# Optimization experiments

Measured on AMD Instinct MI355X. Metric: run time of the kernel, lower is better.

The kernel has to match this reference:

```python
import jax, jax.numpy as jnp
import numpy as np

B, H, W, D, C, NH = 2, 32, 32, 32, 256, 8
LN_EPS = 1e-3  # keras LayerNormalization default epsilon


def _ln(x, g, b):
    m = jnp.mean(x, axis=-1, keepdims=True)
    v = jnp.mean(jnp.square(x - m), axis=-1, keepdims=True)
    return (x - m) * jax.lax.rsqrt(v + LN_EPS) * g + b


def setup_inputs() -> dict:
    key = jax.random.key(0)
    ks = jax.random.split(key, 8)
    w = lambda k, shape, fan: (jax.random.normal(k, shape, jnp.float32) / np.sqrt(fan)).astype(jnp.float32)
    return {
        "q": jax.random.normal(ks[0], (B, H, W, D, C), jnp.float32),
        "kv": jax.random.normal(ks[1], (B, H, W, D, C), jnp.float32),
        "wq_w": w(ks[2], (C, C), C), "wq_b": jnp.zeros((C,), jnp.float32),
        "wk_w": w(ks[3], (C, C), C), "wk_b": jnp.zeros((C,), jnp.float32),
        "wv_w": w(ks[4], (C, C), C), "wv_b": jnp.zeros((C,), jnp.float32),
        "ln1_g": jnp.ones((C,), jnp.float32), "ln1_b": jnp.zeros((C,), jnp.float32),
        "ff1_w": w(ks[5], (C, 4 * C), C), "ff1_b": jnp.zeros((4 * C,), jnp.float32),
        "ff2_w": w(ks[6], (4 * C, C), 4 * C), "ff2_b": jnp.zeros((C,), jnp.float32),
        "ln2_g": jnp.ones((C,), jnp.float32), "ln2_b": jnp.zeros((C,), jnp.float32),
    }


def reference(q, kv, wq_w, wq_b, wk_w, wk_b, wv_w, wv_b,
              ln1_g, ln1_b, ff1_w, ff1_b, ff2_w, ff2_b, ln2_g, ln2_b):
    Bq, Hh, Ww, Dd, Cc = q.shape
    dh = Cc // NH
    qf = q.reshape(Bq, -1, Cc)          # (B, N, C), N = H*W*D
    inq = qf
    kvf = kv.reshape(Bq, -1, Cc)

    def split_heads(x):                  # (B, N, C) -> (B, h, N, dh)
        return x.reshape(Bq, -1, NH, dh).transpose(0, 2, 1, 3)

    qh = split_heads(qf @ wq_w + wq_b)
    kh = split_heads(kvf @ wk_w + wk_b)
    vh = split_heads(kvf @ wv_w + wv_b)

    # efficient (linear) attention: softmax over N on k^T, softmax over dh on q
    k_norm = jax.nn.softmax(kh.transpose(0, 1, 3, 2), axis=-1)   # (B, h, dh, N)
    q_norm = jax.nn.softmax(qh, axis=-1)                         # (B, h, N, dh)
    context = jnp.einsum('bhdn,bhne->bhde', k_norm, vh)          # (B, h, dh, dh)
    attn = jnp.einsum('bhnd,bhde->bhne', q_norm, context)        # (B, h, N, dh)
    attn = attn.transpose(0, 2, 1, 3).reshape(Bq, -1, Cc)

    x = _ln(inq + attn, ln1_g, ln1_b)
    ff = jax.nn.gelu(x @ ff1_w + ff1_b, approximate=False) @ ff2_w + ff2_b
    out = _ln(x + ff, ln2_g, ln2_b)
    return out.reshape(Bq, Hh, Ww, Dd, Cc)
```

## Files before the change

### kernel.cpp

```cpp
#include <hip/hip_runtime.h>
#include <hip/hip_bf16.h>

#define NTOK_B   32768
#define TOK_TOT  65536
#define CDIM     256
#define NHEAD    8
#define DHEAD    32
#define FFDIM    1024
#define LN_EPS   1e-3f

typedef __attribute__((ext_vector_type(8))) short bf16x8;
typedef __attribute__((ext_vector_type(4))) float f32x4;

__device__ __forceinline__ float bf2f(short s) {
    union { unsigned u; float f; } v; v.u = ((unsigned)(unsigned short)s) << 16; return v.f;
}
__device__ __forceinline__ short f2bf(float f) {
    union { float f; unsigned u; } v; v.f = f;
    unsigned r = (v.u + 0x7FFFu + ((v.u >> 16) & 1u)) >> 16;
    return (short)r;
}

__device__ __forceinline__ void gld_lds16(const void* g, void* l) {
    __builtin_amdgcn_global_load_lds(
        (const __attribute__((address_space(1))) unsigned int*)g,
        (__attribute__((address_space(3))) unsigned int*)l, 16, 0, 0);
}

__global__ __launch_bounds__(256) void cast_bf16(const float* __restrict__ in,
                                                 short* __restrict__ out)
{
    long i = ((long)blockIdx.x * 256 + threadIdx.x) * 8;
    float4 a = *(const float4*)(in + i);
    float4 b = *(const float4*)(in + i + 4);
    short t[8];
    t[0] = f2bf(a.x); t[1] = f2bf(a.y); t[2] = f2bf(a.z); t[3] = f2bf(a.w);
    t[4] = f2bf(b.x); t[5] = f2bf(b.y); t[6] = f2bf(b.z); t[7] = f2bf(b.w);
    *(int4*)(out + i) = *(const int4*)t;
}

__global__ __launch_bounds__(256) void transpose_k(const float* __restrict__ in,
                                                   short* __restrict__ out, int K, int N)
{
    __shared__ float t[32][33];
    int kt = blockIdx.x * 32, nt = blockIdx.y * 32;
    int tx = threadIdx.x, ty = threadIdx.y;
#pragma unroll
    for (int i = 0; i < 4; ++i)
        t[ty + i * 8][tx] = in[(long)(kt + ty + i * 8) * N + nt + tx];
    __syncthreads();
#pragma unroll
    for (int i = 0; i < 4; ++i)
        out[(long)(nt + ty + i * 8) * K + kt + tx] = f2bf(t[tx][ty + i * 8]);
}

__global__ __launch_bounds__(256) void concat_bias(const float* __restrict__ a,
                                                   const float* __restrict__ b,
                                                   float* __restrict__ o)
{
    int i = blockIdx.x * 256 + threadIdx.x;
    o[i] = (i < 256) ? a[i] : b[i - 256];
}

template<int ACT, int NBX>
__global__ __launch_bounds__(256) void gemm_bt(const short* __restrict__ Xv,
                                               const short* __restrict__ Wt,
                                               const float* __restrict__ bias,
                                               short* __restrict__ Outp,
                                               int N, int K, int ldx, int ldo)
{
    constexpr int LOG2NBX = (NBX == 2) ? 1 : (NBX == 4) ? 2 : 3;
    __shared__ __align__(16) char smem[49152];
    short* As = (short*)smem;
    short* Bs = (short*)(smem + 24576);

    const int tid  = threadIdx.x;
    const int lane = tid & 63;
    const int wave = tid >> 6;
    const int wm   = (wave >> 1) * 4;
    const int wn   = (wave & 1) * 4;

    const int bid  = blockIdx.x;
    const int xcd  = bid & 7;
    const int j    = bid >> 3;
    const int nblk = j & (NBX - 1);
    const int mblk = xcd * 64 + (j >> LOG2NBX);
    const long m0  = (long)mblk * 128;
    const int  n0  = nblk * 128;

    f32x4 acc[4][4];
#pragma unroll
    for (int i = 0; i < 4; ++i)
#pragma unroll
        for (int jj = 0; jj < 4; ++jj) acc[i][jj] = (f32x4)0.0f;

    const int NT = K >> 5;

    auto stage = [&](int kt, int buf) {
#pragma unroll
        for (int p = 0; p < 2; ++p) {
            int idx = tid + p * 256;
            int row = (idx >> 6) * 16 + (idx & 15);
            int qq  = (idx >> 4) & 3;
            int lofs = buf * 4096 + (p * 256 + wave * 64) * 8;
            gld_lds16(Xv + (m0 + row) * (long)ldx + kt * 32 + qq * 8, As + lofs);
            gld_lds16(Wt + (long)(n0 + row) * K + kt * 32 + qq * 8,  Bs + lofs);
        }
    };

    stage(0, 0);
    if (NT > 1) stage(1, 1);
    int cb = 0;
    for (int kt = 0; kt < NT; ++kt) {
        __builtin_amdgcn_sched_barrier(0);
        if (kt + 1 < NT) asm volatile("s_waitcnt vmcnt(4)" ::: "memory");
        else             asm volatile("s_waitcnt vmcnt(0)" ::: "memory");
        __builtin_amdgcn_s_barrier();
        __builtin_amdgcn_sched_barrier(0);
        if (kt + 2 < NT) {
            int sb = cb + 2; if (sb >= 3) sb -= 3;
            stage(kt + 2, sb);
        }
        bf16x8 a[4], b[4];
#pragma unroll
        for (int i = 0; i < 4; ++i) a[i] = *(const bf16x8*)(As + cb * 4096 + ((wm + i) * 64 + lane) * 8);
#pragma unroll
        for (int jj = 0; jj < 4; ++jj) b[jj] = *(const bf16x8*)(Bs + cb * 4096 + ((wn + jj) * 64 + lane) * 8);
#pragma unroll
        for (int i = 0; i < 4; ++i)
#pragma unroll
            for (int jj = 0; jj < 4; ++jj)
                acc[i][jj] = __builtin_amdgcn_mfma_f32_16x16x32_bf16(a[i], b[jj], acc[i][jj], 0, 0, 0);
        cb = (cb + 1 == 3) ? 0 : cb + 1;
    }

    __syncthreads();
    short* Cs = (short*)smem;
    const int crow0 = (wave >> 1) * 64 + (lane >> 4) * 4;
    const int ccol0 = (wave & 1) * 64 + (lane & 15);
#pragma unroll
    for (int jj = 0; jj < 4; ++jj) {
        int colw = ccol0 + jj * 16;
        float bb = bias[n0 + colw];
#pragma unroll
        for (int i = 0; i < 4; ++i) {
#pragma unroll
            for (int r = 0; r < 4; ++r) {
                float v = acc[i][jj][r] + bb;
                if (ACT == 1) {
                    float w = -1.5957691216057308f * (v + 0.044715f * v * v * v);
                    v = v / (1.0f + __expf(w));
                }
                Cs[(crow0 + i * 16 + r) * 136 + colw] = f2bf(v);
            }
        }
    }
    __syncthreads();
#pragma unroll
    for (int it = 0; it < 8; ++it) {
        int ch = tid + it * 256;
        int row = ch >> 4, c8 = ch & 15;
        int4 v = *(const int4*)(Cs + row * 136 + c8 * 8);
        *(int4*)(Outp + (m0 + row) * (long)ldo + n0 + c8 * 8) = v;
    }
}

__global__ __launch_bounds__(256) void ff2_ln(const short* __restrict__ H,
                                              const short* __restrict__ Wt2,
                                              const float* __restrict__ b2f,
                                              const short* __restrict__ xbuf,
                                              const float* __restrict__ g2,
                                              const float* __restrict__ b2,
                                              float* __restrict__ y)
{
    __shared__ __align__(16) char smem[61440];

    const int tid  = threadIdx.x;
    const int lane = tid & 63;
    const int wave = tid >> 6;

    const int bid  = blockIdx.x;
    const int mblk = (bid & 7) * 128 + (bid >> 3);
    const long m0  = (long)mblk * 64;

    f32x4 acc[4][4];
#pragma unroll
    for (int i = 0; i < 4; ++i)
#pragma unroll
        for (int jj = 0; jj < 4; ++jj) acc[i][jj] = (f32x4)0.0f;

    auto stage = [&](int kt, int buf) {
        char* base = smem + buf * 20480;
        {
            int row = wave * 16 + (lane & 15);
            int qq  = lane >> 4;
            gld_lds16(H + (m0 + row) * 1024L + kt * 32 + qq * 8,
                      base + wave * 1024);
        }
#pragma unroll
        for (int p = 0; p < 4; ++p) {
            int ti  = p * 4 + wave;
            int row = ti * 16 + (lane & 15);
            int qq  = lane >> 4;
            gld_lds16(Wt2 + row * 1024L + kt * 32 + qq * 8,
                      base + 4096 + (p * 256 + wave * 64) * 16);
        }
    };

    const int NT = 32;
    stage(0, 0);
    stage(1, 1);
    int cb = 0;
    for (int kt = 0; kt < NT; ++kt) {
        __builtin_amdgcn_sched_barrier(0);
        if (kt + 1 < NT) asm volatile("s_waitcnt vmcnt(5)" ::: "memory");
        else             asm volatile("s_waitcnt vmcnt(0)" ::: "memory");
        __builtin_amdgcn_s_barrier();
        __builtin_amdgcn_sched_barrier(0);
        if (kt + 2 < NT) {
            int sb = cb + 2; if (sb >= 3) sb -= 3;
            stage(kt + 2, sb);
        }
        const short* Ab = (const short*)(smem + cb * 20480);
        const short* Bb = (const short*)(smem + cb * 20480 + 4096);
        bf16x8 a[4], b[4];
#pragma unroll
        for (int i = 0; i < 4; ++i) a[i] = *(const bf16x8*)(Ab + (i * 64 + lane) * 8);
#pragma unroll
        for (int jj = 0; jj < 4; ++jj) b[jj] = *(const bf16x8*)(Bb + ((wave * 4 + jj) * 64 + lane) * 8);
#pragma unroll
        for (int i = 0; i < 4; ++i)
#pragma unroll
            for (int jj = 0; jj < 4; ++jj)
                acc[i][jj] = __builtin_amdgcn_mfma_f32_16x16x32_bf16(a[i], b[jj], acc[i][jj], 0, 0, 0);
        cb = (cb + 1 == 3) ? 0 : cb + 1;
    }

    __syncthreads();
    float* red = (float*)smem;
    float* mr  = red + 512;

    float g2c[4], b2c[4], bfc[4];
#pragma unroll
    for (int jj = 0; jj < 4; ++jj) {
        int col = wave * 64 + (lane & 15) + jj * 16;
        bfc[jj] = b2f[col]; g2c[jj] = g2[col]; b2c[jj] = b2[col];
    }

#pragma unroll
    for (int i = 0; i < 4; ++i) {
#pragma unroll
        for (int r = 0; r < 4; ++r) {
            int row = i * 16 + (lane >> 4) * 4 + r;
            float s = 0.0f, ss = 0.0f;
#pragma unroll
            for (int jj = 0; jj < 4; ++jj) {
                int col = wave * 64 + (lane & 15) + jj * 16;
                float val = acc[i][jj][r] + bfc[jj]
                          + bf2f(xbuf[(m0 + row) * 256 + col]);
                acc[i][jj][r] = val;
                s += val; ss += val * val;
            }
            s  += __shfl_xor(s, 1);  ss += __shfl_xor(ss, 1);
            s  += __shfl_xor(s, 2);  ss += __shfl_xor(ss, 2);
            s  += __shfl_xor(s, 4);  ss += __shfl_xor(ss, 4);
            s  += __shfl_xor(s, 8);  ss += __shfl_xor(ss, 8);
            if ((lane & 15) == 0) {
                red[(row * 4 + wave) * 2]     = s;
                red[(row * 4 + wave) * 2 + 1] = ss;
            }
        }
    }
    __syncthreads();
    if (tid < 64) {
        float s  = red[tid * 8] + red[tid * 8 + 2] + red[tid * 8 + 4] + red[tid * 8 + 6];
        float ss = red[tid * 8 + 1] + red[tid * 8 + 3] + red[tid * 8 + 5] + red[tid * 8 + 7];
        float mean = s * (1.0f / 256.0f);
        float var  = ss * (1.0f / 256.0f) - mean * mean;
        mr[tid * 2]     = mean;
        mr[tid * 2 + 1] = rsqrtf(var + LN_EPS);
    }
    __syncthreads();
#pragma unroll
    for (int i = 0; i < 4; ++i) {
#pragma unroll
        for (int r = 0; r < 4; ++r) {
            int row = i * 16 + (lane >> 4) * 4 + r;
            float mean = mr[row * 2], rstd = mr[row * 2 + 1];
#pragma unroll
            for (int jj = 0; jj < 4; ++jj) {
                int col = wave * 64 + (lane & 15) + jj * 16;
                y[(m0 + row) * 256 + col] =
                    (acc[i][jj][r] - mean) * rstd * g2c[jj] + b2c[jj];
            }
        }
    }
}

#define CCH 512
#define CPS 64
__global__ __launch_bounds__(256) void context_k(const short* __restrict__ QKV,
                                                 float* __restrict__ ctx,
                                                 float* __restrict__ ksum)
{
    const int b = blockIdx.z, h = blockIdx.y;
    const long tokbase = (long)b * NTOK_B + (long)blockIdx.x * CCH;
    __shared__ __align__(16) float kb[2][CPS][32];
    __shared__ __align__(16) float vb[2][CPS][32];
    const int tid  = threadIdx.x;
    const int wave = tid >> 6;
    const int lane = tid & 63;
    const int t    = lane;
    const int koff = (wave < 2) ? 256 : 512;
    const int choff = (wave & 1) * 16;
    const short* src0 = QKV + (tokbase + t) * 768 + koff + h * 32 + choff;

    const int d2 = lane >> 2;
    const int eg = lane & 3;
    __align__(16) float acc[2][8];
#pragma unroll
    for (int i = 0; i < 2; ++i)
#pragma unroll
        for (int j = 0; j < 8; ++j) acc[i][j] = 0.0f;
    float s0 = 0.0f, s1 = 0.0f;

    int4 p0 = *(const int4*)src0;
    int4 p1 = *(const int4*)(src0 + 8);
    const int NP = CCH / CPS;
    for (int p = 0; p < NP; ++p) {
        int4 n0 = p0, n1 = p1;
        if (p + 1 < NP) {
            const short* sn = src0 + (long)(p + 1) * CPS * 768;
            n0 = *(const int4*)sn;
            n1 = *(const int4*)(sn + 8);
        }
        {
            short sh[16];
            *(int4*)&sh[0] = p0; *(int4*)&sh[8] = p1;
            float v[16];
            if (wave < 2) {
#pragma unroll
                for (int i = 0; i < 16; ++i) v[i] = __expf(bf2f(sh[i]));
            } else {
#pragma unroll
                for (int i = 0; i < 16; ++i) v[i] = bf2f(sh[i]);
            }
            char* rowp = (char*)((wave < 2) ? &kb[p & 1][t][0] : &vb[p & 1][t][0]);
            int sw = (t & 7) << 4;
#pragma unroll
            for (int q = 0; q < 4; ++q) {
                int qq = (choff >> 2) + q;
                *(float4*)(rowp + ((qq * 16) ^ sw)) =
                    make_float4(v[q * 4], v[q * 4 + 1], v[q * 4 + 2], v[q * 4 + 3]);
            }
        }
        __syncthreads();
        {
            const int buf = p & 1;
#pragma unroll
            for (int k = 0; k < 16; ++k) {
                int tt = wave * 16 + k;
                int sw = (tt & 7) << 4;
                const char* krow = (const char*)&kb[buf][tt][0];
                const char* vrow = (const char*)&vb[buf][tt][0];
                float2 kd = *(const float2*)(krow + ((d2 * 8) ^ sw));
                float4 va = *(const float4*)(vrow + ((eg * 32) ^ sw));
                float4 vbb = *(const float4*)(vrow + ((eg * 32 + 16) ^ sw));
                acc[0][0] += kd.x * va.x;  acc[0][1] += kd.x * va.y;
                acc[0][2] += kd.x * va.z;  acc[0][3] += kd.x * va.w;
                acc[0][4] += kd.x * vbb.x; acc[0][5] += kd.x * vbb.y;
                acc[0][6] += kd.x * vbb.z; acc[0][7] += kd.x * vbb.w;
                acc[1][0] += kd.y * va.x;  acc[1][1] += kd.y * va.y;
                acc[1][2] += kd.y * va.z;  acc[1][3] += kd.y * va.w;
                acc[1][4] += kd.y * vbb.x; acc[1][5] += kd.y * vbb.y;
                acc[1][6] += kd.y * vbb.z; acc[1][7] += kd.y * vbb.w;
                if (eg == 0) { s0 += kd.x; s1 += kd.y; }
            }
        }
        p0 = n0; p1 = n1;
    }

    __syncthreads();
    float* red = &kb[0][0][0];
    float* rs  = &vb[0][0][0];
#pragma unroll
    for (int dd = 0; dd < 2; ++dd) {
        *(float4*)&red[wave * 1024 + (d2 * 2 + dd) * 32 + eg * 8]     = *(float4*)&acc[dd][0];
        *(float4*)&red[wave * 1024 + (d2 * 2 + dd) * 32 + eg * 8 + 4] = *(float4*)&acc[dd][4];
    }
    if (eg == 0) { rs[wave * 32 + d2 * 2] = s0; rs[wave * 32 + d2 * 2 + 1] = s1; }
    __syncthreads();
    {
        float* cbase = ctx + ((long)(b * 8 + h) * 32) * 32;
        int i0 = tid * 4;
        float4 a  = *(float4*)&red[i0];
        float4 b4 = *(float4*)&red[1024 + i0];
        float4 c4 = *(float4*)&red[2048 + i0];
        float4 d4 = *(float4*)&red[3072 + i0];
        atomicAdd(cbase + i0 + 0, a.x + b4.x + c4.x + d4.x);
        atomicAdd(cbase + i0 + 1, a.y + b4.y + c4.y + d4.y);
        atomicAdd(cbase + i0 + 2, a.z + b4.z + c4.z + d4.z);
        atomicAdd(cbase + i0 + 3, a.w + b4.w + c4.w + d4.w);
        if (tid < 32) {
            float s = rs[tid] + rs[32 + tid] + rs[64 + tid] + rs[96 + tid];
            atomicAdd(ksum + b * 256 + h * 32 + tid, s);
        }
    }
}

__global__ __launch_bounds__(256) void attn_ln1(const short* __restrict__ QKV,
                                                const float* __restrict__ qin,
                                                const float* __restrict__ ctx,
                                                const float* __restrict__ ksum,
                                                const float* __restrict__ g1,
                                                const float* __restrict__ b1,
                                                short* __restrict__ xout)
{
    long tok0blk = (long)blockIdx.x * 128;
    int b = (int)(tok0blk >> 15);
    __shared__ __align__(16) float qn[16][292];
    __shared__ __align__(16) float xb[16][292];
    __shared__ float red[16][8][2];
    __shared__ float mr[16][2];
    int tid = threadIdx.x;
    int h = tid >> 5, e = tid & 31;

    float cregs[32];
    {
        const float* cp = ctx + ((long)(b * 8 + h) * 32) * 32 + e;
        const float* zs = ksum + b * 256 + h * 32;
#pragma unroll
        for (int d = 0; d < 32; ++d) cregs[d] = cp[d * 32] / zs[d];
    }

    for (int sub = 0; sub < 8; ++sub) {
        long tok0 = tok0blk + sub * 16;
        if (tid < 128) {
            int tA = tid >> 3, hA = tid & 7;
            const short* Qp = QKV + (tok0 + tA) * 768 + hA * 32;
            short qv[32];
            *(int4*)&qv[0]  = *(const int4*)(Qp);
            *(int4*)&qv[8]  = *(const int4*)(Qp + 8);
            *(int4*)&qv[16] = *(const int4*)(Qp + 16);
            *(int4*)&qv[24] = *(const int4*)(Qp + 24);
            float f[32]; float mx = -1e30f;
#pragma unroll
            for (int i = 0; i < 32; ++i) { f[i] = bf2f(qv[i]); mx = fmaxf(mx, f[i]); }
            float s = 0.0f;
#pragma unroll
            for (int i = 0; i < 32; ++i) { f[i] = __expf(f[i] - mx); s += f[i]; }
            float inv = 1.0f / s;
            float* qrow = &qn[tA][hA * 36];
#pragma unroll
            for (int i = 0; i < 32; ++i) qrow[i] = f[i] * inv;
        }
        __syncthreads();
        {
            int cch = h * 32 + e;
#pragma unroll 2
            for (int t = 0; t < 16; ++t) {
                const float4* qr = (const float4*)&qn[t][h * 36];
                float a = 0.0f;
#pragma unroll
                for (int d4 = 0; d4 < 8; ++d4) {
                    float4 qv = qr[d4];
                    a += qv.x * cregs[d4 * 4 + 0] + qv.y * cregs[d4 * 4 + 1]
                       + qv.z * cregs[d4 * 4 + 2] + qv.w * cregs[d4 * 4 + 3];
                }
                float iv = qin[(tok0 + t) * 256 + cch];
                xb[t][cch] = a + iv;
            }
        }
        __syncthreads();
        if (tid < 128) {
            int tC = tid & 15, sC = tid >> 4;
            float s = 0, ss = 0;
            const float* xr = &xb[tC][sC * 32];
#pragma unroll
            for (int i = 0; i < 32; ++i) { float v = xr[i]; s += v; ss += v * v; }
            red[tC][sC][0] = s; red[tC][sC][1] = ss;
        }
        __syncthreads();
        if (tid < 16) {
            float s = 0, ss = 0;
#pragma unroll
            for (int k = 0; k < 8; ++k) { s += red[tid][k][0]; ss += red[tid][k][1]; }
            float mean = s * (1.0f / 256.0f);
            float var  = ss * (1.0f / 256.0f) - mean * mean;
            mr[tid][0] = mean; mr[tid][1] = rsqrtf(var + LN_EPS);
        }
        __syncthreads();
        if (tid < 128) {
            int tC = tid & 15, sC = tid >> 4;
            float mean = mr[tC][0], rstd = mr[tC][1];
            const float* xr = &xb[tC][sC * 32];
            short ov[32];
#pragma unroll
            for (int i = 0; i < 32; ++i) {
                int c = sC * 32 + i;
                float v = (xr[i] - mean) * rstd * g1[c] + b1[c];
                ov[i] = f2bf(v);
            }
            int4* op = (int4*)(xout + (tok0 + tC) * 256 + sC * 32);
            op[0] = *(int4*)&ov[0];  op[1] = *(int4*)&ov[8];
            op[2] = *(int4*)&ov[16]; op[3] = *(int4*)&ov[24];
        }
        __syncthreads();
    }
}

extern "C" void kernel_launch(void* const* d_in, const int* in_sizes, int n_in,
                              void* d_out, int out_size, void* d_ws, size_t ws_size,
                              hipStream_t stream)
{
    const float* q    = (const float*)d_in[0];
    const float* kv   = (const float*)d_in[1];
    const float* wq_w = (const float*)d_in[2];
    const float* wq_b = (const float*)d_in[3];
    const float* wk_w = (const float*)d_in[4];
    const float* wk_b = (const float*)d_in[5];
    const float* wv_w = (const float*)d_in[6];
    const float* wv_b = (const float*)d_in[7];
    const float* ln1g = (const float*)d_in[8];
    const float* ln1b = (const float*)d_in[9];
    const float* ff1w = (const float*)d_in[10];
    const float* ff1b = (const float*)d_in[11];
    const float* ff2w = (const float*)d_in[12];
    const float* ff2b = (const float*)d_in[13];
    const float* ln2g = (const float*)d_in[14];
    const float* ln2b = (const float*)d_in[15];

    char* w = (char*)d_ws;
    short* Wtq = (short*)w; w += 131072;
    short* Wtk = (short*)w; w += 131072;
    short* Wtv = (short*)w; w += 131072;
    short* Wt1 = (short*)w; w += 524288;
    short* Wt2 = (short*)w; w += 524288;
    float* ksm = (float*)w; w += 2048;
    float* bkv = (float*)w; w += 2048;
    float* ctx = (float*)w; w += 65536;
    short* xbuf= (short*)w; w += 33554432;
    short* QKV = (short*)w; w += 134217728;
    short* kvb = (short*)w; w += 33554432;
    short* h1  = QKV;
    short* qb  = xbuf;
    float* y   = (float*)d_out;

    cast_bf16<<<8192, 256, 0, stream>>>(q,  qb);
    cast_bf16<<<8192, 256, 0, stream>>>(kv, kvb);

    dim3 tb(32, 8);
    transpose_k<<<dim3(8, 8),  tb, 0, stream>>>(wq_w, Wtq, 256, 256);
    transpose_k<<<dim3(8, 8),  tb, 0, stream>>>(wk_w, Wtk, 256, 256);
    transpose_k<<<dim3(8, 8),  tb, 0, stream>>>(wv_w, Wtv, 256, 256);
    transpose_k<<<dim3(8, 32), tb, 0, stream>>>(ff1w, Wt1, 256, 1024);
    transpose_k<<<dim3(32, 8), tb, 0, stream>>>(ff2w, Wt2, 1024, 256);
    concat_bias<<<2, 256, 0, stream>>>(wk_b, wv_b, bkv);

    gemm_bt<0,2><<<1024, 256, 0, stream>>>(qb,  Wtq, wq_b, QKV + 0,   256, 256, 256, 768);
    gemm_bt<0,4><<<2048, 256, 0, stream>>>(kvb, Wtk, bkv,  QKV + 256, 512, 256, 256, 768);

    hipMemsetAsync(ctx, 0, 65536, stream);
    hipMemsetAsync(ksm, 0, 2048, stream);
    context_k<<<dim3(NTOK_B / CCH, 8, 2), 256, 0, stream>>>(QKV, ctx, ksm);

    attn_ln1<<<512, 256, 0, stream>>>(QKV, q, ctx, ksm, ln1g, ln1b, xbuf);

    gemm_bt<1,8><<<4096, 256, 0, stream>>>(xbuf, Wt1, ff1b, h1, 1024, 256, 256, 1024);

    ff2_ln<<<1024, 256, 0, stream>>>(h1, Wt2, ff2b, xbuf, ln2g, ln2b, y);
}
```

Before: 570.5 us.

## Fuse FF1 GEMM, GELU, FF2 GEMM and LayerNorm into one kernel

```diff
diff --git a/kernel.cpp b/kernel.cpp
--- a/kernel.cpp
+++ b/kernel.cpp
@@ -25,6 +25,11 @@
     __builtin_amdgcn_global_load_lds(
         (const __attribute__((address_space(1))) unsigned int*)g,
         (__attribute__((address_space(3))) unsigned int*)l, 16, 0, 0);
+}
+
+__device__ __forceinline__ float fast_gelu(float v) {
+    float w = -1.5957691216057308f * (v + 0.044715f * v * v * v);
+    return v / (1.0f + __expf(w));
 }
 
 __global__ __launch_bounds__(256) void cast_bf16(const float* __restrict__ in,
@@ -147,10 +152,7 @@
 #pragma unroll
             for (int r = 0; r < 4; ++r) {
                 float v = acc[i][jj][r] + bb;
-                if (ACT == 1) {
-                    float w = -1.5957691216057308f * (v + 0.044715f * v * v * v);
-                    v = v / (1.0f + __expf(w));
-                }
+                if (ACT == 1) v = fast_gelu(v);
                 Cs[(crow0 + i * 16 + r) * 136 + colw] = f2bf(v);
             }
         }
@@ -165,85 +167,131 @@
     }
 }
 
-__global__ __launch_bounds__(256) void ff2_ln(const short* __restrict__ H,
-                                              const short* __restrict__ Wt2,
-                                              const float* __restrict__ b2f,
-                                              const short* __restrict__ xbuf,
-                                              const float* __restrict__ g2,
-                                              const float* __restrict__ b2,
-                                              float* __restrict__ y)
-{
-    __shared__ __align__(16) char smem[61440];
+__global__ __launch_bounds__(256, 2) void ffn_fused(const short* __restrict__ X,
+                                                    const short* __restrict__ W1t,
+                                                    const float* __restrict__ b1f,
+                                                    const short* __restrict__ W2t,
+                                                    const float* __restrict__ b2f,
+                                                    const short* __restrict__ xdummy,
+                                                    const float* __restrict__ g2,
+                                                    const float* __restrict__ b2,
+                                                    float* __restrict__ y)
+{
+    __shared__ __align__(16) short lds[40960];
+    short* Xs = lds;
+    short* Wb = lds + 16384;
+    short* hs = lds + 32768;
 
     const int tid  = threadIdx.x;
     const int lane = tid & 63;
-    const int wave = tid >> 6;
+    const int w    = tid >> 6;
 
     const int bid  = blockIdx.x;
     const int mblk = (bid & 7) * 128 + (bid >> 3);
     const long m0  = (long)mblk * 64;
 
-    f32x4 acc[4][4];
+    f32x4 yacc[4][4];
 #pragma unroll
     for (int i = 0; i < 4; ++i)
 #pragma unroll
-        for (int jj = 0; jj < 4; ++jj) acc[i][jj] = (f32x4)0.0f;
-
-    auto stage = [&](int kt, int buf) {
-        char* base = smem + buf * 20480;
-        {
-            int row = wave * 16 + (lane & 15);
-            int qq  = lane >> 4;
-            gld_lds16(H + (m0 + row) * 1024L + kt * 32 + qq * 8,
-                      base + wave * 1024);
-        }
+        for (int jj = 0; jj < 4; ++jj) yacc[i][jj] = (f32x4)0.0f;
+
+    {
+        int ti = (tid >> 6) & 3, q = (tid >> 4) & 3, m = tid & 15;
+        const short* gsrc = X + (m0 + ti * 16 + m) * 256 + q * 8;
+#pragma unroll
+        for (int it = 0; it < 8; ++it)
+            gld_lds16(gsrc + it * 32, Xs + it * 2048 + w * 512);
+    }
+
+    auto stageW1 = [&](int c, int s, int buf) {
+#pragma unroll
+        for (int p = 0; p < 2; ++p) {
+            int cc = p * 256 + tid;
+            int ti = cc >> 6, q = (cc >> 4) & 3, m = cc & 15;
+            gld_lds16(W1t + (c * 128 + ti * 16 + m) * 256 + s * 32 + q * 8,
+                      Wb + buf * 8192 + (p * 256 + w * 64) * 8);
+        }
+    };
+    auto stageW2 = [&](int c, int ks, int buf) {
 #pragma unroll
         for (int p = 0; p < 4; ++p) {
-            int ti  = p * 4 + wave;
-            int row = ti * 16 + (lane & 15);
-            int qq  = lane >> 4;
-            gld_lds16(Wt2 + row * 1024L + kt * 32 + qq * 8,
-                      base + 4096 + (p * 256 + wave * 64) * 16);
+            int cc = p * 256 + tid;
+            int ti = cc >> 6, q = (cc >> 4) & 3, m = cc & 15;
+            gld_lds16(W2t + (ti * 16 + m) * 1024 + c * 128 + ks * 32 + q * 8,
+                      Wb + buf * 8192 + (p * 256 + w * 64) * 8);
         }
     };
 
-    const int NT = 32;
-    stage(0, 0);
-    stage(1, 1);
-    int cb = 0;
-    for (int kt = 0; kt < NT; ++kt) {
-        __builtin_amdgcn_sched_barrier(0);
-        if (kt + 1 < NT) asm volatile("s_waitcnt vmcnt(5)" ::: "memory");
-        else             asm volatile("s_waitcnt vmcnt(0)" ::: "memory");
-        __builtin_amdgcn_s_barrier();
-        __builtin_amdgcn_sched_barrier(0);
-        if (kt + 2 < NT) {
-            int sb = cb + 2; if (sb >= 3) sb -= 3;
-            stage(kt + 2, sb);
-        }
-        const short* Ab = (const short*)(smem + cb * 20480);
-        const short* Bb = (const short*)(smem + cb * 20480 + 4096);
-        bf16x8 a[4], b[4];
-#pragma unroll
-        for (int i = 0; i < 4; ++i) a[i] = *(const bf16x8*)(Ab + (i * 64 + lane) * 8);
-#pragma unroll
-        for (int jj = 0; jj < 4; ++jj) b[jj] = *(const bf16x8*)(Bb + ((wave * 4 + jj) * 64 + lane) * 8);
-#pragma unroll
-        for (int i = 0; i < 4; ++i)
-#pragma unroll
-            for (int jj = 0; jj < 4; ++jj)
-                acc[i][jj] = __builtin_amdgcn_mfma_f32_16x16x32_bf16(a[i], b[jj], acc[i][jj], 0, 0, 0);
-        cb = (cb + 1 == 3) ? 0 : cb + 1;
-    }
-
-    __syncthreads();
-    float* red = (float*)smem;
+    stageW1(0, 0, 0);
+
+    f32x4 hacc[4][2];
+    float b1a = 0.0f, b1b = 0.0f;
+
+    for (int c = 0; c < 8; ++c) {
+#pragma unroll
+        for (int u = 0; u < 12; ++u) {
+            __syncthreads();
+            if (u == 0) {
+                b1a = b1f[c * 128 + w * 32 + (lane & 15)];
+                b1b = b1f[c * 128 + w * 32 + 16 + (lane & 15)];
+#pragma unroll
+                for (int i = 0; i < 4; ++i) { hacc[i][0] = (f32x4)0.0f; hacc[i][1] = (f32x4)0.0f; }
+            }
+            if (u + 1 < 8)        stageW1(c, u + 1, (u + 1) & 1);
+            else if (u + 1 < 12)  stageW2(c, u + 1 - 8, (u + 1) & 1);
+            else if (c + 1 < 8)   stageW1(c + 1, 0, 0);
+
+            const short* Wc = Wb + (u & 1) * 8192;
+            if (u < 8) {
+                bf16x8 a[4], b[2];
+#pragma unroll
+                for (int i = 0; i < 4; ++i) a[i] = *(const bf16x8*)(Xs + u * 2048 + (i * 64 + lane) * 8);
+#pragma unroll
+                for (int jj = 0; jj < 2; ++jj) b[jj] = *(const bf16x8*)(Wc + ((w * 2 + jj) * 64 + lane) * 8);
+#pragma unroll
+                for (int i = 0; i < 4; ++i)
+#pragma unroll
+                    for (int jj = 0; jj < 2; ++jj)
+                        hacc[i][jj] = __builtin_amdgcn_mfma_f32_16x16x32_bf16(a[i], b[jj], hacc[i][jj], 0, 0, 0);
+                if (u == 7) {
+#pragma unroll
+                    for (int jj = 0; jj < 2; ++jj) {
+                        int q = jj * 2 + ((lane >> 3) & 1);
+                        float bb = jj ? b1b : b1a;
+#pragma unroll
+                        for (int i = 0; i < 4; ++i)
+#pragma unroll
+                            for (int r = 0; r < 4; ++r) {
+                                float v = fast_gelu(hacc[i][jj][r] + bb);
+                                hs[w * 2048 + (i * 64 + q * 16 + (lane >> 4) * 4 + r) * 8 + (lane & 7)] = f2bf(v);
+                            }
+                    }
+                }
+            } else {
+                const int ks = u - 8;
+                bf16x8 a[4], b[4];
+#pragma unroll
+                for (int i = 0; i < 4; ++i) a[i] = *(const bf16x8*)(hs + ks * 2048 + (i * 64 + lane) * 8);
+#pragma unroll
+                for (int jj = 0; jj < 4; ++jj) b[jj] = *(const bf16x8*)(Wc + ((w * 4 + jj) * 64 + lane) * 8);
+#pragma unroll
+                for (int i = 0; i < 4; ++i)
+#pragma unroll
+                    for (int jj = 0; jj < 4; ++jj)
+                        yacc[i][jj] = __builtin_amdgcn_mfma_f32_16x16x32_bf16(a[i], b[jj], yacc[i][jj], 0, 0, 0);
+            }
+        }
+    }
+
+    __syncthreads();
+    float* red = (float*)hs;
     float* mr  = red + 512;
 
     float g2c[4], b2c[4], bfc[4];
 #pragma unroll
     for (int jj = 0; jj < 4; ++jj) {
-        int col = wave * 64 + (lane & 15) + jj * 16;
+        int col = w * 64 + (lane & 15) + jj * 16;
         bfc[jj] = b2f[col]; g2c[jj] = g2[col]; b2c[jj] = b2[col];
     }
 
@@ -255,10 +303,11 @@
             float s = 0.0f, ss = 0.0f;
 #pragma unroll
             for (int jj = 0; jj < 4; ++jj) {
-                int col = wave * 64 + (lane & 15) + jj * 16;
-                float val = acc[i][jj][r] + bfc[jj]
-                          + bf2f(xbuf[(m0 + row) * 256 + col]);
-                acc[i][jj][r] = val;
+                int kt = w * 2 + (jj >> 1);
+                int q  = 2 * (jj & 1) + ((lane >> 3) & 1);
+                short xres = Xs[kt * 2048 + (i * 64 + q * 16 + (lane >> 4) * 4 + r) * 8 + (lane & 7)];
+                float val = yacc[i][jj][r] + bfc[jj] + bf2f(xres);
+                yacc[i][jj][r] = val;
                 s += val; ss += val * val;
             }
             s  += __shfl_xor(s, 1);  ss += __shfl_xor(ss, 1);
@@ -266,8 +315,8 @@
             s  += __shfl_xor(s, 4);  ss += __shfl_xor(ss, 4);
             s  += __shfl_xor(s, 8);  ss += __shfl_xor(ss, 8);
             if ((lane & 15) == 0) {
-                red[(row * 4 + wave) * 2]     = s;
-                red[(row * 4 + wave) * 2 + 1] = ss;
+                red[(row * 4 + w) * 2]     = s;
+                red[(row * 4 + w) * 2 + 1] = ss;
             }
         }
     }
@@ -289,9 +338,9 @@
             float mean = mr[row * 2], rstd = mr[row * 2 + 1];
 #pragma unroll
             for (int jj = 0; jj < 4; ++jj) {
-                int col = wave * 64 + (lane & 15) + jj * 16;
+                int col = w * 64 + (lane & 15) + jj * 16;
                 y[(m0 + row) * 256 + col] =
-                    (acc[i][jj][r] - mean) * rstd * g2c[jj] + b2c[jj];
+                    (yacc[i][jj][r] - mean) * rstd * g2c[jj] + b2c[jj];
             }
         }
     }
@@ -542,7 +591,6 @@
     short* xbuf= (short*)w; w += 33554432;
     short* QKV = (short*)w; w += 134217728;
     short* kvb = (short*)w; w += 33554432;
-    short* h1  = QKV;
     short* qb  = xbuf;
     float* y   = (float*)d_out;
 
@@ -566,7 +614,6 @@
 
     attn_ln1<<<512, 256, 0, stream>>>(QKV, q, ctx, ksm, ln1g, ln1b, xbuf);
 
-    gemm_bt<1,8><<<4096, 256, 0, stream>>>(xbuf, Wt1, ff1b, h1, 1024, 256, 256, 1024);
-
-    ff2_ln<<<1024, 256, 0, stream>>>(h1, Wt2, ff2b, xbuf, ln2g, ln2b, y);
-}
+    ffn_fused<<<1024, 256, 0, stream>>>(xbuf, Wt1, ff1b, Wt2, ff2b, xbuf,
+                                        ln2g, ln2b, y);
+}
```

Result: faster. 552.9 us (-3.1%).
